# Optimization experiments

Hardware: AMD Instinct MI355X
Metric: run time of the kernel (lower is better)

The kernel has to match this reference:

```python
import jax, jax.numpy as jnp
import numpy as np
import math

B, C, H, W = 4, 256, 64, 64
N_GROUPS = 32
D_K = 64
N_HEADS = C // D_K  # 4
EPS = 1e-5


def setup_inputs() -> dict:
    key = jax.random.key(0)
    ks = jax.random.split(key, 7)
    return {
        "x": jax.random.normal(ks[0], (B, C, H, W), dtype=jnp.float32),
        "gamma": jax.random.uniform(ks[1], (C,), dtype=jnp.float32),
        "beta": jax.random.normal(ks[2], (C,), dtype=jnp.float32) * 0.1,
        "W_qkv": jax.random.normal(ks[3], (C, N_HEADS * D_K * 3), dtype=jnp.float32) * 0.02,
        "b_qkv": jax.random.normal(ks[4], (N_HEADS * D_K * 3,), dtype=jnp.float32) * 0.02,
        "W_out": jax.random.normal(ks[5], (N_HEADS * D_K, C), dtype=jnp.float32) * 0.02,
        "b_out": jax.random.normal(ks[6], (C,), dtype=jnp.float32) * 0.02,
    }


def _group_norm(x, gamma, beta):
    # x: [B, C, H, W], 32 groups, biased variance, eps=1e-5 (torch GroupNorm defaults)
    b, c, h, w = x.shape
    xg = x.reshape(b, N_GROUPS, c // N_GROUPS, h, w)
    mean = jnp.mean(xg, axis=(2, 3, 4), keepdims=True)
    var = jnp.var(xg, axis=(2, 3, 4), keepdims=True)
    xn = (xg - mean) / jnp.sqrt(var + EPS)
    xn = xn.reshape(b, c, h, w)
    return xn * gamma[None, :, None, None] + beta[None, :, None, None]


def reference(x, gamma, beta, W_qkv, b_qkv, W_out, b_out):
    b, c, h, w = x.shape
    n = h * w
    scale = 1.0 / math.sqrt(math.sqrt(D_K))
    # norm -> [B, N, C]
    hid = _group_norm(x, gamma, beta).reshape(b, c, n).transpose(0, 2, 1)
    # qkv projection -> [B, N, n_heads, 3*d_k], chunk on last dim
    qkv = (hid @ W_qkv + b_qkv).reshape(b, n, N_HEADS, 3 * D_K)
    q, k, v = jnp.split(qkv, 3, axis=-1)  # each [B, N, H, d_k]
    attn = jnp.einsum('bihd,bjhd->bijh', q * scale, k * scale)
    attn = jax.nn.softmax(attn, axis=2)  # softmax over j (keys)
    res = jnp.einsum('bijh,bjhd->bihd', attn, v).reshape(b, n, N_HEADS * D_K)
    res = res @ W_out + b_out  # [B, N, C]
    res = res.transpose(0, 2, 1).reshape(b, c, h, w)
    return (res + x) / math.sqrt(2.0)
```

## Files before the change

### kernel.cpp

```cpp
#include <hip/hip_runtime.h>
#include <math.h>

typedef float  f32x4   __attribute__((ext_vector_type(4)));
typedef float  f32x16  __attribute__((ext_vector_type(16)));
typedef __bf16 bf16x8  __attribute__((ext_vector_type(8)));
typedef __bf16 bf16x4  __attribute__((ext_vector_type(4)));

#define MFMA16(a, b, c) __builtin_amdgcn_mfma_f32_16x16x32_bf16((a), (b), (c), 0, 0, 0)
#define MFMA32(a, b, c) __builtin_amdgcn_mfma_f32_32x32x16_bf16((a), (b), (c), 0, 0, 0)

#define TRR(dst, a, lit)  asm volatile("ds_read_b64_tr_b16 %0, %1 offset:" lit : "=v"(dst) : "v"(a))
#define TRRM(dst, a, lit) asm volatile("ds_read_b64_tr_b16 %0, %1 offset:" lit : "=v"(dst) : "v"(a) : "memory")
#define SHUF8(a, b) __builtin_shufflevector((a), (b), 0, 1, 2, 3, 4, 5, 6, 7)

typedef __attribute__((address_space(3))) unsigned int lds_u32;
typedef __attribute__((address_space(1))) const unsigned int glb_u32;

__device__ __forceinline__ void gload16(const __bf16* g, char* l) {
    __builtin_amdgcn_global_load_lds((glb_u32*)g, (lds_u32*)l, 16, 0, 0);
}

static constexpr int BATCH = 4;
static constexpr int CH    = 256;
static constexpr int M_TOT = BATCH * 4096;

static constexpr float QSCALE = 0.18033688011112042f;

static constexpr size_t OFF_WQKV  = 0;
static constexpr size_t OFF_WOUT  = 196608ull * 2;
static constexpr size_t OFF_STATS = OFF_WOUT + 65536ull * 2;
static constexpr size_t OFF_HID   = OFF_STATS + 1024;
static constexpr size_t OFF_Q     = OFF_HID + (size_t)M_TOT * CH * 2;
static constexpr size_t OFF_K     = OFF_Q   + (size_t)M_TOT * CH * 2;
static constexpr size_t OFF_V     = OFF_K   + (size_t)M_TOT * CH * 2;

__global__ __launch_bounds__(256) void pre_kernel(const float* __restrict__ x,
                                                  float2* __restrict__ stats,
                                                  const float* __restrict__ wq,
                                                  const float* __restrict__ wo,
                                                  __bf16* __restrict__ wqf,
                                                  __bf16* __restrict__ wof) {
    if (blockIdx.x < 128) {
        int bg = blockIdx.x;
        const float4* p = (const float4*)(x + (size_t)bg * 32768);
        float s = 0.f, ss = 0.f;
        for (int i = threadIdx.x; i < 8192; i += 256) {
            float4 v = p[i];
            s  += (v.x + v.y) + (v.z + v.w);
            ss += v.x * v.x + v.y * v.y + v.z * v.z + v.w * v.w;
        }
#pragma unroll
        for (int d = 32; d > 0; d >>= 1) { s += __shfl_down(s, d); ss += __shfl_down(ss, d); }
        __shared__ float sh[8];
        int w = threadIdx.x >> 6, l = threadIdx.x & 63;
        if (l == 0) { sh[w] = s; sh[4 + w] = ss; }
        __syncthreads();
        if (threadIdx.x == 0) {
            float S = sh[0] + sh[1] + sh[2] + sh[3];
            float SS = sh[4] + sh[5] + sh[6] + sh[7];
            float mean = S * (1.f / 32768.f);
            float var  = SS * (1.f / 32768.f) - mean * mean;
            stats[bg] = make_float2(mean, rsqrtf(var + 1e-5f));
        }
    } else {
        int i = (blockIdx.x - 128) * 256 + threadIdx.x;
        if (i < 196608) {
            int e = i & 7, l = (i >> 3) & 63, kk = (i >> 9) & 7, jt = i >> 12;
            int kidx = kk * 32 + ((l >> 4) << 3) + e;
            int n = jt * 16 + (l & 15);
            wqf[i] = (__bf16)wq[kidx * 768 + n];
        } else {
            int i2 = i - 196608;
            int e = i2 & 7, l = (i2 >> 3) & 63, kk = (i2 >> 9) & 7, jt = i2 >> 12;
            int kidx = kk * 32 + ((l >> 4) << 3) + e;
            int n = jt * 16 + (l & 15);
            wof[i2] = (__bf16)wo[kidx * 256 + n];
        }
    }
}

__global__ __launch_bounds__(256) void gn_apply(const float* __restrict__ x,
                                                const float* __restrict__ gamma,
                                                const float* __restrict__ beta,
                                                const float2* __restrict__ stats,
                                                __bf16* __restrict__ hid) {
    int b  = blockIdx.x >> 6;
    int n0 = (blockIdx.x & 63) << 6;
    int c  = threadIdx.x;
    float2 st = stats[b * 32 + (c >> 3)];
    float gm = gamma[c] * st.y;
    float bt = beta[c] - st.x * gm;
    const float* xp = x + ((size_t)(b * 256 + c)) * 4096 + n0;
    __bf16* hp = hid + ((size_t)(b * 4096 + n0)) * 256 + c;
#pragma unroll
    for (int j4 = 0; j4 < 16; ++j4) {
        float4 v = *(const float4*)(xp + j4 * 4);
        hp[(size_t)(j4 * 4 + 0) * 256] = (__bf16)(v.x * gm + bt);
        hp[(size_t)(j4 * 4 + 1) * 256] = (__bf16)(v.y * gm + bt);
        hp[(size_t)(j4 * 4 + 2) * 256] = (__bf16)(v.z * gm + bt);
        hp[(size_t)(j4 * 4 + 3) * 256] = (__bf16)(v.w * gm + bt);
    }
}

__global__ __launch_bounds__(256) void qkv_gemm(const __bf16* __restrict__ hid,
                                                const __bf16* __restrict__ wf,
                                                const float* __restrict__ bqkv,
                                                __bf16* __restrict__ qb,
                                                __bf16* __restrict__ kb,
                                                __bf16* __restrict__ vb) {
    const int mt = blockIdx.x, nt = blockIdx.y;
    const int tid = threadIdx.x;
    const int w = tid >> 6, l = tid & 63;
    const int lr = l & 15, lh = l >> 4;
    f32x4 acc[4] = {{0.f,0.f,0.f,0.f},{0.f,0.f,0.f,0.f},{0.f,0.f,0.f,0.f},{0.f,0.f,0.f,0.f}};
    const __bf16* ap = hid + (size_t)(mt * 64 + w * 16 + lr) * 256 + lh * 8;
#pragma unroll
    for (int kk = 0; kk < 8; ++kk) {
        bf16x8 a = *(const bf16x8*)(ap + kk * 32);
#pragma unroll
        for (int fj = 0; fj < 4; ++fj) {
            bf16x8 bf = *(const bf16x8*)(wf + (size_t)(((nt * 4 + fj) * 8 + kk) * 64 + l) * 8);
            acc[fj] = MFMA16(a, bf, acc[fj]);
        }
    }
    int mbase = mt * 64 + w * 16 + lh * 4;
#pragma unroll
    for (int fj = 0; fj < 4; ++fj) {
        int j = nt * 64 + fj * 16 + lr;
        int head = j / 192, rem = j % 192;
        int part = rem >> 6, dd = rem & 63;
        float bias = bqkv[j];
        float sc = (part == 0) ? QSCALE : 1.0f;
        __bf16* dst = (part == 0) ? qb : (part == 1) ? kb : vb;
#pragma unroll
        for (int r = 0; r < 4; ++r) {
            int m = mbase + r;
            int b = m >> 12, n = m & 4095;
            dst[((size_t)((b * 4 + head) * 4096 + n)) * 64 + dd] = (__bf16)((acc[fj][r] + bias) * sc);
        }
    }
}

__global__ __launch_bounds__(256, 2) void attn_fwd(const __bf16* __restrict__ q,
                                                   const __bf16* __restrict__ k,
                                                   const __bf16* __restrict__ v,
                                                   __bf16* __restrict__ ao) {
    const int id = blockIdx.x;
    const int within = id >> 3;
    const int bh = ((id & 7) << 1) + (within >> 5);
    const int q0 = (within & 31) * 128;
    const int tid = threadIdx.x;
    const int wv = tid >> 6, l = tid & 63;
    const int l31 = l & 31, h = l >> 5;

    __shared__ __attribute__((aligned(16))) char smem[32768];

    const size_t base = (size_t)bh * (4096 * 64);

    const int c0 = wv * 64 + l;
    const int rK = c0 >> 3, cbK = l & 7;
    const int gk0 = rK * 64 + (cbK ^ (rK & 7)) * 8;
    const int gk1 = gk0 + 2048;
    auto vsrc = [](int c) -> int {
        int u = c >> 5, r6 = (c >> 3) & 3, j = (c >> 1) & 3, d8 = c & 1;
        int kstep = u >> 2, dt = (u >> 1) & 1, eh = u & 1;
        int kt = kstep >> 1, s = kstep & 1;
        int hq = r6 >> 1, hh = r6 & 1, e = eh * 4 + j;
        int key = kt * 32 + s * 16 + (e >> 2) * 8 + hq * 4 + (e & 3);
        return key * 64 + dt * 32 + hh * 16 + d8 * 8;
    };
    const int gv0 = vsrc(c0), gv1 = vsrc(c0 + 256);
    const int lw0 = wv * 1024;
    const int lw1 = 4096 + wv * 1024;

    const __bf16* kg = k + base;
    const __bf16* vg = v + base;

    const unsigned lanep = (unsigned)((l & 15) * 2 + (l >> 4) * 128);
    const unsigned vA0 = (unsigned)(size_t)(smem + 16384) + lanep;
    const unsigned vA1 = vA0 + 8192u;

    int koff[2][4];
#pragma unroll
    for (int kt = 0; kt < 2; ++kt) {
        int row = kt * 32 + l31;
#pragma unroll
        for (int ks = 0; ks < 4; ++ks)
            koff[kt][ks] = row * 128 + ((ks * 32 + h * 16) ^ ((row & 7) << 4));
    }

    bf16x8 qf[4];
    {
        const __bf16* qp = q + base + (size_t)(q0 + wv * 32 + l31) * 64 + h * 8;
#pragma unroll
        for (int ks = 0; ks < 4; ++ks) qf[ks] = *(const bf16x8*)(qp + ks * 16);
    }
    bf16x8 ones;
#pragma unroll
    for (int e = 0; e < 8; ++e) ones[e] = (__bf16)1.0f;

    f32x16 O0 = (f32x16)0.0f, O1 = (f32x16)0.0f, LS = (f32x16)0.0f;

    gload16(kg + gk0, smem + lw0);
    gload16(kg + gk1, smem + lw1);
    gload16(vg + gv0, smem + 16384 + lw0);
    gload16(vg + gv1, smem + 16384 + lw1);
    __syncthreads();

    auto body = [&](const char* Kc, unsigned vA, char* kd, char* vd, int tnext) {
        if (tnext < 64) {
            const __bf16* kp = kg + (size_t)tnext * 4096;
            const __bf16* vp = vg + (size_t)tnext * 4096;
            gload16(kp + gk0, kd + lw0);
            gload16(kp + gk1, kd + lw1);
            gload16(vp + gv0, vd + lw0);
            gload16(vp + gv1, vd + lw1);
        }

        f32x16 S0 = (f32x16)0.0f, S1 = (f32x16)0.0f;
        __builtin_amdgcn_s_setprio(1);
#pragma unroll
        for (int ks = 0; ks < 4; ++ks) {
            bf16x8 ka0 = *(const bf16x8*)(Kc + koff[0][ks]);
            bf16x8 ka1 = *(const bf16x8*)(Kc + koff[1][ks]);
            S0 = MFMA32(ka0, qf[ks], S0);
            S1 = MFMA32(ka1, qf[ks], S1);
        }
        __builtin_amdgcn_s_setprio(0);

        bf16x4 u0, u1, u2, u3, u4, u5, u6, u7, u8, u9, u10, u11, u12, u13, u14, u15;
        TRRM(u0,  vA, "0");    TRR(u1,  vA, "512");
        TRR(u2,  vA, "1024");  TRR(u3,  vA, "1536");
        TRR(u4,  vA, "2048");  TRR(u5,  vA, "2560");
        TRR(u6,  vA, "3072");  TRR(u7,  vA, "3584");
        TRR(u8,  vA, "4096");  TRR(u9,  vA, "4608");
        TRR(u10, vA, "5120");  TRR(u11, vA, "5632");
        TRR(u12, vA, "6144");  TRR(u13, vA, "6656");
        TRR(u14, vA, "7168");  TRR(u15, vA, "7680");

        bf16x8 B0, B1, B2, B3;
#pragma unroll
        for (int e = 0; e < 8; ++e) {
            B0[e] = (__bf16)__builtin_amdgcn_exp2f(S0[e]);
            B1[e] = (__bf16)__builtin_amdgcn_exp2f(S0[8 + e]);
            B2[e] = (__bf16)__builtin_amdgcn_exp2f(S1[e]);
            B3[e] = (__bf16)__builtin_amdgcn_exp2f(S1[8 + e]);
        }

        asm volatile("s_waitcnt lgkmcnt(0)" ::: "memory");
        __builtin_amdgcn_sched_barrier(0);
        __builtin_amdgcn_s_setprio(1);
        O0 = MFMA32(SHUF8(u0,  u1),  B0, O0);
        O1 = MFMA32(SHUF8(u2,  u3),  B0, O1);
        LS = MFMA32(ones, B0, LS);
        O0 = MFMA32(SHUF8(u4,  u5),  B1, O0);
        O1 = MFMA32(SHUF8(u6,  u7),  B1, O1);
        LS = MFMA32(ones, B1, LS);
        O0 = MFMA32(SHUF8(u8,  u9),  B2, O0);
        O1 = MFMA32(SHUF8(u10, u11), B2, O1);
        LS = MFMA32(ones, B2, LS);
        O0 = MFMA32(SHUF8(u12, u13), B3, O0);
        O1 = MFMA32(SHUF8(u14, u15), B3, O1);
        LS = MFMA32(ones, B3, LS);
        __builtin_amdgcn_s_setprio(0);

        __syncthreads();
    };

    for (int t = 0; t < 64; t += 2) {
        body(smem,        vA0, smem + 8192, smem + 16384 + 8192, t + 1);
        body(smem + 8192, vA1, smem,        smem + 16384,        t + 2);
    }

    float inv = 1.0f / LS[0];
    int b = bh >> 2, hd = bh & 3;
    int n = q0 + wv * 32 + l31;
    __bf16* dst = ao + ((size_t)(b * 4096 + n)) * 256 + hd * 64 + h * 4;
#pragma unroll
    for (int dt = 0; dt < 2; ++dt) {
        const f32x16& O = dt ? O1 : O0;
#pragma unroll
        for (int g = 0; g < 4; ++g) {
            bf16x4 pk;
#pragma unroll
            for (int m = 0; m < 4; ++m) pk[m] = (__bf16)(O[g * 4 + m] * inv);
            *(bf16x4*)(dst + dt * 32 + g * 8) = pk;
        }
    }
}

__global__ __launch_bounds__(256) void out_gemm(const __bf16* __restrict__ ao,
                                                const __bf16* __restrict__ wf,
                                                const float* __restrict__ bout,
                                                const float* __restrict__ x,
                                                float* __restrict__ out) {
    const int mt = blockIdx.x, nt = blockIdx.y;
    const int tid = threadIdx.x;
    const int w = tid >> 6, l = tid & 63;
    const int lr = l & 15, lh = l >> 4;
    f32x4 acc[4] = {{0.f,0.f,0.f,0.f},{0.f,0.f,0.f,0.f},{0.f,0.f,0.f,0.f},{0.f,0.f,0.f,0.f}};
    const __bf16* ap = ao + (size_t)(mt * 64 + w * 16 + lr) * 256 + lh * 8;
#pragma unroll
    for (int kk = 0; kk < 8; ++kk) {
        bf16x8 a = *(const bf16x8*)(ap + kk * 32);
#pragma unroll
        for (int fj = 0; fj < 4; ++fj) {
            bf16x8 bf = *(const bf16x8*)(wf + (size_t)(((nt * 4 + fj) * 8 + kk) * 64 + l) * 8);
            acc[fj] = MFMA16(a, bf, acc[fj]);
        }
    }
    __shared__ float tile[64][72];
#pragma unroll
    for (int fj = 0; fj < 4; ++fj) {
        float bias = bout[nt * 64 + fj * 16 + lr];
#pragma unroll
        for (int r = 0; r < 4; ++r)
            tile[w * 16 + lh * 4 + r][fj * 16 + lr] = acc[fj][r] + bias;
    }
    __syncthreads();
    int b  = mt >> 6;
    int n0 = (mt & 63) * 64;
    int c0 = nt * 64;
    int cl = tid >> 2, nq = tid & 3;
    size_t gbase = ((size_t)(b * 256 + c0 + cl)) * 4096 + n0 + nq * 16;
#pragma unroll
    for (int i = 0; i < 16; i += 4) {
        float4 xv = *(const float4*)(x + gbase + i);
        float4 ov;
        ov.x = (tile[nq * 16 + i + 0][cl] + xv.x) * 0.70710678118654752f;
        ov.y = (tile[nq * 16 + i + 1][cl] + xv.y) * 0.70710678118654752f;
        ov.z = (tile[nq * 16 + i + 2][cl] + xv.z) * 0.70710678118654752f;
        ov.w = (tile[nq * 16 + i + 3][cl] + xv.w) * 0.70710678118654752f;
        *(float4*)(out + gbase + i) = ov;
    }
}

extern "C" void kernel_launch(void* const* d_in, const int* in_sizes, int n_in,
                              void* d_out, int out_size, void* d_ws, size_t ws_size,
                              hipStream_t stream) {
    const float* x     = (const float*)d_in[0];
    const float* gamma = (const float*)d_in[1];
    const float* beta  = (const float*)d_in[2];
    const float* W_qkv = (const float*)d_in[3];
    const float* b_qkv = (const float*)d_in[4];
    const float* W_out = (const float*)d_in[5];
    const float* b_out = (const float*)d_in[6];
    float* out = (float*)d_out;
    char* ws = (char*)d_ws;

    __bf16* wqf   = (__bf16*)(ws + OFF_WQKV);
    __bf16* wof   = (__bf16*)(ws + OFF_WOUT);
    float2* stats = (float2*)(ws + OFF_STATS);
    __bf16* hid   = (__bf16*)(ws + OFF_HID);
    __bf16* qb    = (__bf16*)(ws + OFF_Q);
    __bf16* kb    = (__bf16*)(ws + OFF_K);
    __bf16* vb    = (__bf16*)(ws + OFF_V);

    pre_kernel<<<1152, 256, 0, stream>>>(x, stats, W_qkv, W_out, wqf, wof);
    gn_apply<<<256, 256, 0, stream>>>(x, gamma, beta, stats, hid);
    qkv_gemm<<<dim3(256, 12), 256, 0, stream>>>(hid, wqf, b_qkv, qb, kb, vb);
    attn_fwd<<<512, 256, 0, stream>>>(qb, kb, vb, hid);
    out_gemm<<<dim3(256, 4), 256, 0, stream>>>(hid, wof, b_out, x, out);
}
```

Before: 143.7 us.

## Store V transposed from QKV GEMM and read it with plain LDS loads

```diff
diff --git a/kernel.cpp b/kernel.cpp
--- a/kernel.cpp
+++ b/kernel.cpp
@@ -8,10 +8,6 @@
 
 #define MFMA16(a, b, c) __builtin_amdgcn_mfma_f32_16x16x32_bf16((a), (b), (c), 0, 0, 0)
 #define MFMA32(a, b, c) __builtin_amdgcn_mfma_f32_32x32x16_bf16((a), (b), (c), 0, 0, 0)
-
-#define TRR(dst, a, lit)  asm volatile("ds_read_b64_tr_b16 %0, %1 offset:" lit : "=v"(dst) : "v"(a))
-#define TRRM(dst, a, lit) asm volatile("ds_read_b64_tr_b16 %0, %1 offset:" lit : "=v"(dst) : "v"(a) : "memory")
-#define SHUF8(a, b) __builtin_shufflevector((a), (b), 0, 1, 2, 3, 4, 5, 6, 7)
 
 typedef __attribute__((address_space(3))) unsigned int lds_u32;
 typedef __attribute__((address_space(1))) const unsigned int glb_u32;
@@ -123,27 +119,54 @@
             acc[fj] = MFMA16(a, bf, acc[fj]);
         }
     }
-    int mbase = mt * 64 + w * 16 + lh * 4;
-#pragma unroll
-    for (int fj = 0; fj < 4; ++fj) {
-        int j = nt * 64 + fj * 16 + lr;
-        int head = j / 192, rem = j % 192;
-        int part = rem >> 6, dd = rem & 63;
-        float bias = bqkv[j];
-        float sc = (part == 0) ? QSCALE : 1.0f;
-        __bf16* dst = (part == 0) ? qb : (part == 1) ? kb : vb;
-#pragma unroll
-        for (int r = 0; r < 4; ++r) {
-            int m = mbase + r;
-            int b = m >> 12, n = m & 4095;
-            dst[((size_t)((b * 4 + head) * 4096 + n)) * 64 + dd] = (__bf16)((acc[fj][r] + bias) * sc);
+    const int part = nt % 3;
+    const int head = nt / 3;
+    const int b  = mt >> 6;
+    const int n0 = (mt & 63) * 64;
+
+    if (part == 2) {
+        __shared__ float tile[64][72];
+#pragma unroll
+        for (int fj = 0; fj < 4; ++fj) {
+            float bias = bqkv[head * 192 + 128 + fj * 16 + lr];
+#pragma unroll
+            for (int r = 0; r < 4; ++r)
+                tile[w * 16 + lh * 4 + r][fj * 16 + lr] = acc[fj][r] + bias;
+        }
+        __syncthreads();
+        int dd = tid >> 2, nq = tid & 3;
+        __bf16* dstrow = vb + ((size_t)((b * 4 + head) * 64 + dd)) * 4096 + n0 + nq * 16;
+        bf16x8 w0, w1;
+#pragma unroll
+        for (int cc = 0; cc < 8; ++cc) {
+            int nl0 = nq * 16 + 8 * ((cc >> 2) & 1) + 4 * (cc >> 3) + (cc & 3);
+            int cc1 = cc + 8;
+            int nl1 = nq * 16 + 8 * ((cc1 >> 2) & 1) + 4 * (cc1 >> 3) + (cc1 & 3);
+            w0[cc] = (__bf16)tile[nl0][dd];
+            w1[cc] = (__bf16)tile[nl1][dd];
+        }
+        *(bf16x8*)dstrow = w0;
+        *(bf16x8*)(dstrow + 8) = w1;
+    } else {
+        __bf16* dst = (part == 0) ? qb : kb;
+        const float sc = (part == 0) ? QSCALE : 1.0f;
+        int mbase = w * 16 + lh * 4;
+#pragma unroll
+        for (int fj = 0; fj < 4; ++fj) {
+            int dd = fj * 16 + lr;
+            float bias = bqkv[head * 192 + part * 64 + dd];
+#pragma unroll
+            for (int r = 0; r < 4; ++r) {
+                int n = n0 + mbase + r;
+                dst[((size_t)((b * 4 + head) * 4096 + n)) * 64 + dd] = (__bf16)((acc[fj][r] + bias) * sc);
+            }
         }
     }
 }
 
 __global__ __launch_bounds__(256, 2) void attn_fwd(const __bf16* __restrict__ q,
                                                    const __bf16* __restrict__ k,
-                                                   const __bf16* __restrict__ v,
+                                                   const __bf16* __restrict__ vt,
                                                    __bf16* __restrict__ ao) {
     const int id = blockIdx.x;
     const int within = id >> 3;
@@ -161,32 +184,21 @@
     const int rK = c0 >> 3, cbK = l & 7;
     const int gk0 = rK * 64 + (cbK ^ (rK & 7)) * 8;
     const int gk1 = gk0 + 2048;
-    auto vsrc = [](int c) -> int {
-        int u = c >> 5, r6 = (c >> 3) & 3, j = (c >> 1) & 3, d8 = c & 1;
-        int kstep = u >> 2, dt = (u >> 1) & 1, eh = u & 1;
-        int kt = kstep >> 1, s = kstep & 1;
-        int hq = r6 >> 1, hh = r6 & 1, e = eh * 4 + j;
-        int key = kt * 32 + s * 16 + (e >> 2) * 8 + hq * 4 + (e & 3);
-        return key * 64 + dt * 32 + hh * 16 + d8 * 8;
-    };
-    const int gv0 = vsrc(c0), gv1 = vsrc(c0 + 256);
+    const int gv0 = rK * 4096 + (cbK ^ (rK & 7)) * 8;
+    const int gv1 = gv0 + 32 * 4096;
     const int lw0 = wv * 1024;
     const int lw1 = 4096 + wv * 1024;
 
     const __bf16* kg = k + base;
-    const __bf16* vg = v + base;
-
-    const unsigned lanep = (unsigned)((l & 15) * 2 + (l >> 4) * 128);
-    const unsigned vA0 = (unsigned)(size_t)(smem + 16384) + lanep;
-    const unsigned vA1 = vA0 + 8192u;
-
-    int koff[2][4];
-#pragma unroll
-    for (int kt = 0; kt < 2; ++kt) {
-        int row = kt * 32 + l31;
-#pragma unroll
-        for (int ks = 0; ks < 4; ++ks)
-            koff[kt][ks] = row * 128 + ((ks * 32 + h * 16) ^ ((row & 7) << 4));
+    const __bf16* vg = vt + base;
+
+    int foff[2][4];
+#pragma unroll
+    for (int b32 = 0; b32 < 2; ++b32) {
+        int row = b32 * 32 + l31;
+#pragma unroll
+        for (int s = 0; s < 4; ++s)
+            foff[b32][s] = row * 128 + ((s * 32 + h * 16) ^ ((row & 7) << 4));
     }
 
     bf16x8 qf[4];
@@ -207,10 +219,10 @@
     gload16(vg + gv1, smem + 16384 + lw1);
     __syncthreads();
 
-    auto body = [&](const char* Kc, unsigned vA, char* kd, char* vd, int tnext) {
+    auto body = [&](const char* Kc, const char* Vc, char* kd, char* vd, int tnext) {
         if (tnext < 64) {
             const __bf16* kp = kg + (size_t)tnext * 4096;
-            const __bf16* vp = vg + (size_t)tnext * 4096;
+            const __bf16* vp = vg + (size_t)tnext * 64;
             gload16(kp + gk0, kd + lw0);
             gload16(kp + gk1, kd + lw1);
             gload16(vp + gv0, vd + lw0);
@@ -221,22 +233,12 @@
         __builtin_amdgcn_s_setprio(1);
 #pragma unroll
         for (int ks = 0; ks < 4; ++ks) {
-            bf16x8 ka0 = *(const bf16x8*)(Kc + koff[0][ks]);
-            bf16x8 ka1 = *(const bf16x8*)(Kc + koff[1][ks]);
+            bf16x8 ka0 = *(const bf16x8*)(Kc + foff[0][ks]);
+            bf16x8 ka1 = *(const bf16x8*)(Kc + foff[1][ks]);
             S0 = MFMA32(ka0, qf[ks], S0);
             S1 = MFMA32(ka1, qf[ks], S1);
         }
         __builtin_amdgcn_s_setprio(0);
-
-        bf16x4 u0, u1, u2, u3, u4, u5, u6, u7, u8, u9, u10, u11, u12, u13, u14, u15;
-        TRRM(u0,  vA, "0");    TRR(u1,  vA, "512");
-        TRR(u2,  vA, "1024");  TRR(u3,  vA, "1536");
-        TRR(u4,  vA, "2048");  TRR(u5,  vA, "2560");
-        TRR(u6,  vA, "3072");  TRR(u7,  vA, "3584");
-        TRR(u8,  vA, "4096");  TRR(u9,  vA, "4608");
-        TRR(u10, vA, "5120");  TRR(u11, vA, "5632");
-        TRR(u12, vA, "6144");  TRR(u13, vA, "6656");
-        TRR(u14, vA, "7168");  TRR(u15, vA, "7680");
 
         bf16x8 B0, B1, B2, B3;
 #pragma unroll
@@ -247,29 +249,37 @@
             B3[e] = (__bf16)__builtin_amdgcn_exp2f(S1[8 + e]);
         }
 
-        asm volatile("s_waitcnt lgkmcnt(0)" ::: "memory");
-        __builtin_amdgcn_sched_barrier(0);
         __builtin_amdgcn_s_setprio(1);
-        O0 = MFMA32(SHUF8(u0,  u1),  B0, O0);
-        O1 = MFMA32(SHUF8(u2,  u3),  B0, O1);
-        LS = MFMA32(ones, B0, LS);
-        O0 = MFMA32(SHUF8(u4,  u5),  B1, O0);
-        O1 = MFMA32(SHUF8(u6,  u7),  B1, O1);
-        LS = MFMA32(ones, B1, LS);
-        O0 = MFMA32(SHUF8(u8,  u9),  B2, O0);
-        O1 = MFMA32(SHUF8(u10, u11), B2, O1);
-        LS = MFMA32(ones, B2, LS);
-        O0 = MFMA32(SHUF8(u12, u13), B3, O0);
-        O1 = MFMA32(SHUF8(u14, u15), B3, O1);
-        LS = MFMA32(ones, B3, LS);
+        {
+            bf16x8 v00 = *(const bf16x8*)(Vc + foff[0][0]);
+            bf16x8 v10 = *(const bf16x8*)(Vc + foff[1][0]);
+            O0 = MFMA32(v00, B0, O0);
+            O1 = MFMA32(v10, B0, O1);
+            LS = MFMA32(ones, B0, LS);
+            bf16x8 v01 = *(const bf16x8*)(Vc + foff[0][1]);
+            bf16x8 v11 = *(const bf16x8*)(Vc + foff[1][1]);
+            O0 = MFMA32(v01, B1, O0);
+            O1 = MFMA32(v11, B1, O1);
+            LS = MFMA32(ones, B1, LS);
+            bf16x8 v02 = *(const bf16x8*)(Vc + foff[0][2]);
+            bf16x8 v12 = *(const bf16x8*)(Vc + foff[1][2]);
+            O0 = MFMA32(v02, B2, O0);
+            O1 = MFMA32(v12, B2, O1);
+            LS = MFMA32(ones, B2, LS);
+            bf16x8 v03 = *(const bf16x8*)(Vc + foff[0][3]);
+            bf16x8 v13 = *(const bf16x8*)(Vc + foff[1][3]);
+            O0 = MFMA32(v03, B3, O0);
+            O1 = MFMA32(v13, B3, O1);
+            LS = MFMA32(ones, B3, LS);
+        }
         __builtin_amdgcn_s_setprio(0);
 
         __syncthreads();
     };
 
     for (int t = 0; t < 64; t += 2) {
-        body(smem,        vA0, smem + 8192, smem + 16384 + 8192, t + 1);
-        body(smem + 8192, vA1, smem,        smem + 16384,        t + 2);
+        body(smem,        smem + 16384,        smem + 8192, smem + 16384 + 8192, t + 1);
+        body(smem + 8192, smem + 16384 + 8192, smem,        smem + 16384,        t + 2);
     }
 
     float inv = 1.0f / LS[0];
@@ -354,11 +364,11 @@
     __bf16* hid   = (__bf16*)(ws + OFF_HID);
     __bf16* qb    = (__bf16*)(ws + OFF_Q);
     __bf16* kb    = (__bf16*)(ws + OFF_K);
-    __bf16* vb    = (__bf16*)(ws + OFF_V);
+    __bf16* vbt   = (__bf16*)(ws + OFF_V);
 
     pre_kernel<<<1152, 256, 0, stream>>>(x, stats, W_qkv, W_out, wqf, wof);
     gn_apply<<<256, 256, 0, stream>>>(x, gamma, beta, stats, hid);
-    qkv_gemm<<<dim3(256, 12), 256, 0, stream>>>(hid, wqf, b_qkv, qb, kb, vb);
-    attn_fwd<<<512, 256, 0, stream>>>(qb, kb, vb, hid);
+    qkv_gemm<<<dim3(256, 12), 256, 0, stream>>>(hid, wqf, b_qkv, qb, kb, vbt);
+    attn_fwd<<<512, 256, 0, stream>>>(qb, kb, vbt, hid);
     out_gemm<<<dim3(256, 4), 256, 0, stream>>>(hid, wof, b_out, x, out);
 }
```

After: 144.4 us. No clear change (+0.4%).
